# Kernel optimization log

Hardware: AMD Instinct MI355X
Metric: run time of the kernel (lower is better)

## Reference

```python
import jax, jax.numpy as jnp
import numpy as np

N = 50000       # nodes
E = 800000      # edges
NUM_IN, NUM_HID, NUM_OUT = 128, 32, 40
K = 2           # ARMA stacks (both convs)
T = 2           # ARMA layers per conv (shared weights)


def setup_inputs() -> dict:
    key = jax.random.key(0)
    ks = jax.random.split(key, 12)
    def glorot(k, shape, fan_in):
        return jax.random.normal(k, shape, jnp.float32) / np.sqrt(fan_in)
    return {
        "x": jax.random.normal(ks[0], (N, NUM_IN), jnp.float32),
        "edge_index": jax.random.randint(ks[1], (2, E), 0, N, dtype=jnp.int32),
        "w1_init": glorot(ks[2], (K, NUM_IN, NUM_HID), NUM_IN),
        "w1_deep": glorot(ks[3], (K, NUM_HID, NUM_HID), NUM_HID),
        "w1_root": glorot(ks[4], (K, NUM_IN, NUM_HID), NUM_IN),
        "b1": jnp.zeros((K, NUM_HID), jnp.float32),
        "w2_init": glorot(ks[5], (K, NUM_HID, NUM_OUT), NUM_HID),
        "w2_deep": glorot(ks[6], (K, NUM_OUT, NUM_OUT), NUM_OUT),
        "w2_root": glorot(ks[7], (K, NUM_HID, NUM_OUT), NUM_HID),
        "b2": jnp.zeros((K, NUM_OUT), jnp.float32),
    }


def _gcn_norm(row, col, n, dtype):
    # symmetric norm without self loops (PyG ARMAConv default)
    deg = jax.ops.segment_sum(jnp.ones(row.shape[0], dtype), col, num_segments=n)
    dinv = jnp.where(deg > 0, jax.lax.rsqrt(jnp.maximum(deg, 1e-12)), 0.0).astype(dtype)
    return dinv[row] * dinv[col]  # [E]


def _arma_conv(x, row, col, ew, w_init, w_deep, w_root, b, use_act):
    # x: [N, F_in] -> out: [N, F_out]; K stacks, T shared-weight layers
    n = x.shape[0]
    root = jnp.einsum('nf,kfh->nkh', x, w_root)   # [N, K, F_out] (shared root weight)
    out = jnp.einsum('nf,kfh->nkh', x, w_init)
    for t in range(T):
        if t > 0:
            out = jnp.einsum('nkh,khg->nkg', out, w_deep)
        msg = out[row] * ew[:, None, None]         # gather at source, [E, K, F_out]
        out = jax.ops.segment_sum(msg, col, num_segments=n)  # scatter-add at target
        out = out + root + b[None, :, :]
        if use_act:
            out = jax.nn.relu(out)
    return out.mean(axis=1)  # mean over stacks


def reference(x, edge_index, w1_init, w1_deep, w1_root, b1,
              w2_init, w2_deep, w2_root, b2):
    row, col = edge_index[0], edge_index[1]
    ew = _gcn_norm(row, col, x.shape[0], x.dtype)
    h1 = _arma_conv(x, row, col, ew, w1_init, w1_deep, w1_root, b1, use_act=True)
    h = jax.nn.relu(h1)
    h2 = _arma_conv(h, row, col, ew, w2_init, w2_deep, w2_root, b2, use_act=False)
    return jax.nn.log_softmax(h2, axis=1)
```

## Files before the change

kernel.cpp:

```cpp
#include <hip/hip_runtime.h>
#include <math.h>


typedef unsigned short ushort_t;
typedef __attribute__((ext_vector_type(8))) short  short8v;
typedef __attribute__((ext_vector_type(4))) float  float4v;
typedef __attribute__((ext_vector_type(2))) float  f32x2;

__device__ inline ushort_t f2bf(float v) {
    unsigned u = __float_as_uint(v);
    u += 0x7FFFu + ((u >> 16) & 1u);
    return (ushort_t)(u >> 16);
}
__device__ inline f32x2 unpack2(unsigned p) {
    f32x2 r;
    r[0] = __uint_as_float(p << 16);
    r[1] = __uint_as_float(p & 0xFFFF0000u);
    return r;
}

__global__ void k_hist(const int* __restrict__ col, int* __restrict__ deg, int e) {
    int i = blockIdx.x * blockDim.x + threadIdx.x;
    if (i < e) atomicAdd(&deg[col[i]], 1);
}

__global__ void k_dinv(const int* __restrict__ deg, float* __restrict__ dinv, int n) {
    int i = blockIdx.x * blockDim.x + threadIdx.x;
    if (i < n) {
        int d = deg[i];
        dinv[i] = d > 0 ? rsqrtf((float)d) : 0.0f;
    }
}

__global__ void k_scan1(const int* __restrict__ deg, int* __restrict__ start,
                        int* __restrict__ bsum, int n) {
    __shared__ int s[256];
    int t = threadIdx.x, idx = blockIdx.x * 256 + t;
    int v = (idx < n) ? deg[idx] : 0;
    s[t] = v; __syncthreads();
    for (int o = 1; o < 256; o <<= 1) {
        int x = (t >= o) ? s[t - o] : 0;
        __syncthreads(); s[t] += x; __syncthreads();
    }
    if (idx <= n) start[idx] = s[t] - v;
    if (t == 255) bsum[blockIdx.x] = s[255];
}

__global__ void k_scan2(const int* __restrict__ bsum, int* __restrict__ bscan) {
    __shared__ int s[256];
    int t = threadIdx.x;
    int v = bsum[t]; s[t] = v; __syncthreads();
    for (int o = 1; o < 256; o <<= 1) {
        int x = (t >= o) ? s[t - o] : 0;
        __syncthreads(); s[t] += x; __syncthreads();
    }
    bscan[t] = s[t] - v;
}

__global__ void k_scan3(int* __restrict__ start, int* __restrict__ cursor,
                        const int* __restrict__ bscan, int n) {
    int idx = blockIdx.x * 256 + threadIdx.x;
    if (idx <= n) {
        int v = start[idx] + bscan[idx >> 8];
        start[idx] = v;
        if (idx < n) cursor[idx] = v;
    }
}

__global__ void k_sort(const int* __restrict__ row, const int* __restrict__ col,
                       const float* __restrict__ dinv, int* __restrict__ cursor,
                       int2* __restrict__ sedge, int e) {
    int i = blockIdx.x * blockDim.x + threadIdx.x;
    if (i < e) {
        int r = row[i], c = col[i];
        int pos = atomicAdd(&cursor[c], 1);
        sedge[pos] = make_int2(r, __float_as_int(dinv[r] * dinv[c]));
    }
}

__global__ void k_wprep(const float* __restrict__ wi, const float* __restrict__ wr,
                        ushort_t* __restrict__ Wt, int K, int F, int H) {
    int idx = blockIdx.x * blockDim.x + threadIdx.x;
    int tot = 2 * K * H * F;
    if (idx >= tot) return;
    int f = idx % F, colx = idx / F;
    int KH = K * H;
    const float* src = (colx < KH) ? wi : wr;
    int c = (colx < KH) ? colx : colx - KH;
    int k = c / H, h = c % H;
    Wt[idx] = f2bf(src[((long)k * F + f) * H + h]);
}

__global__ void k_wprep_diag(const float* __restrict__ w, ushort_t* __restrict__ Wt,
                             int K, int F, int FPAD) {
    int idx = blockIdx.x * blockDim.x + threadIdx.x;
    int tot = K * F * FPAD;
    if (idx >= tot) return;
    int kin = idx % FPAD, colx = idx / FPAD;
    int k = colx / F, h = colx % F;
    float v = 0.0f;
    if (kin < K * F) {
        int kp = kin / F, f = kin % F;
        if (kp == k) v = w[((long)k * F + f) * F + h];
    }
    Wt[idx] = f2bf(v);
}

template<typename XT, int FIN, int FPAD, int NCOLT, int KF0, bool SPLIT>
__global__ void k_mfma_gemm(const XT* __restrict__ X,
                            const ushort_t* __restrict__ Wt,
                            ushort_t* __restrict__ out0,
                            ushort_t* __restrict__ rootb,
                            int n) {
    constexpr int KSTEPS = FPAD / 32;
    int wid  = (blockIdx.x * blockDim.x + threadIdx.x) >> 6;
    int lane = threadIdx.x & 63;
    int m0 = wid * 16;
    if (m0 >= n) return;
    int r = lane & 15, g = lane >> 4;
    float4v acc[NCOLT];
#pragma unroll
    for (int c = 0; c < NCOLT; ++c) acc[c] = (float4v){0.f, 0.f, 0.f, 0.f};
#pragma unroll
    for (int ks = 0; ks < KSTEPS; ++ks) {
        int kb = ks * 32 + g * 8;
        short8v af;
        if constexpr (sizeof(XT) == 2) {
            af = *(const short8v*)&X[(long)(m0 + r) * FIN + kb];
        } else {
            const float* xr = (const float*)X + (long)(m0 + r) * FIN + kb;
            float4 x0 = *(const float4*)xr;
            float4 x1 = *(const float4*)(xr + 4);
            af[0] = (short)f2bf(x0.x); af[1] = (short)f2bf(x0.y);
            af[2] = (short)f2bf(x0.z); af[3] = (short)f2bf(x0.w);
            af[4] = (short)f2bf(x1.x); af[5] = (short)f2bf(x1.y);
            af[6] = (short)f2bf(x1.z); af[7] = (short)f2bf(x1.w);
        }
#pragma unroll
        for (int c = 0; c < NCOLT; ++c) {
            short8v bf = *(const short8v*)&Wt[(long)(c * 16 + r) * FPAD + kb];
            acc[c] = __builtin_amdgcn_mfma_f32_16x16x32_bf16(af, bf, acc[c], 0, 0, 0);
        }
    }
#pragma unroll
    for (int c = 0; c < NCOLT; ++c) {
        int colx = c * 16 + r;
#pragma unroll
        for (int i = 0; i < 4; ++i) {
            long node = m0 + g * 4 + i;
            ushort_t val = f2bf(acc[c][i]);
            if (!SPLIT || colx < KF0)
                out0[node * KF0 + colx] = val;
            else
                rootb[node * KF0 + (colx - KF0)] = val;
        }
    }
}

template<int LPN, int MODE>
__global__ void k_gatherD(const ushort_t* __restrict__ A, const int2* __restrict__ sedge,
                          const int* __restrict__ start, const ushort_t* __restrict__ root,
                          const float* __restrict__ bias, void* __restrict__ outv,
                          int npairs) {
    const unsigned* A32 = (const unsigned*)A;
    const unsigned* R32 = (const unsigned*)root;
    int gid = blockIdx.x * blockDim.x + threadIdx.x;
    int q = gid / LPN, sub = gid % LPN;
    if (q >= npairs) return;
    int na = 2 * q, nb = 2 * q + 1;
    f32x2 bi = *(const f32x2*)&bias[2 * sub];
    f32x2 acca = unpack2(R32[(long)na * LPN + sub]) + bi;
    f32x2 accb = unpack2(R32[(long)nb * LPN + sub]) + bi;
    int ea = start[na], e1a = start[na + 1];
    int eb = start[nb], e1b = start[nb + 1];
    while (ea < e1a && eb < e1b) {
        int2 pa = sedge[ea]; int2 pb = sedge[eb];
        f32x2 va = unpack2(A32[(long)pa.x * LPN + sub]);
        f32x2 vb = unpack2(A32[(long)pb.x * LPN + sub]);
        float wa = __int_as_float(pa.y), wb = __int_as_float(pb.y);
        acca[0] = fmaf(va[0], wa, acca[0]); acca[1] = fmaf(va[1], wa, acca[1]);
        accb[0] = fmaf(vb[0], wb, accb[0]); accb[1] = fmaf(vb[1], wb, accb[1]);
        ++ea; ++eb;
    }
    for (; ea < e1a; ++ea) {
        int2 p = sedge[ea];
        f32x2 v = unpack2(A32[(long)p.x * LPN + sub]);
        float w = __int_as_float(p.y);
        acca[0] = fmaf(v[0], w, acca[0]); acca[1] = fmaf(v[1], w, acca[1]);
    }
    for (; eb < e1b; ++eb) {
        int2 p = sedge[eb];
        f32x2 v = unpack2(A32[(long)p.x * LPN + sub]);
        float w = __int_as_float(p.y);
        accb[0] = fmaf(v[0], w, accb[0]); accb[1] = fmaf(v[1], w, accb[1]);
    }
    if (MODE == 3) {
        float* out = (float*)outv;
        *(f32x2*)&out[(long)na * 2 * LPN + 2 * sub] = acca;
        *(f32x2*)&out[(long)nb * 2 * LPN + 2 * sub] = accb;
    } else if (MODE == 2) {
        unsigned* out = (unsigned*)outv;
        float a0 = fmaxf(acca[0], 0.f), a1 = fmaxf(acca[1], 0.f);
        float b0 = fmaxf(accb[0], 0.f), b1 = fmaxf(accb[1], 0.f);
        float oa0 = __shfl_xor(a0, 16), oa1 = __shfl_xor(a1, 16);
        float ob0 = __shfl_xor(b0, 16), ob1 = __shfl_xor(b1, 16);
        if (sub < 16) {
            unsigned pka = (unsigned)f2bf(0.5f * (a0 + oa0)) |
                           ((unsigned)f2bf(0.5f * (a1 + oa1)) << 16);
            unsigned pkb = (unsigned)f2bf(0.5f * (b0 + ob0)) |
                           ((unsigned)f2bf(0.5f * (b1 + ob1)) << 16);
            out[(long)na * 16 + sub] = pka;
            out[(long)nb * 16 + sub] = pkb;
        }
    } else {
        unsigned* out = (unsigned*)outv;
        float a0 = acca[0], a1 = acca[1], b0 = accb[0], b1 = accb[1];
        if (MODE == 1) {
            a0 = fmaxf(a0, 0.f); a1 = fmaxf(a1, 0.f);
            b0 = fmaxf(b0, 0.f); b1 = fmaxf(b1, 0.f);
        }
        out[(long)na * LPN + sub] = (unsigned)f2bf(a0) | ((unsigned)f2bf(a1) << 16);
        out[(long)nb * LPN + sub] = (unsigned)f2bf(b0) | ((unsigned)f2bf(b1) << 16);
    }
}

__global__ void k_logsoftmax(const float* __restrict__ B, float* __restrict__ out, int n) {
    int gid  = blockIdx.x * blockDim.x + threadIdx.x;
    int wave = gid >> 6;
    int lane = gid & 63;
    if (wave >= n) return;
    float v = -INFINITY;
    if (lane < 40)
        v = 0.5f * (B[(long)wave * 80 + lane] + B[(long)wave * 80 + 40 + lane]);
    float m = v;
#pragma unroll
    for (int o = 32; o; o >>= 1) m = fmaxf(m, __shfl_xor(m, o));
    float ex = (lane < 40) ? expf(v - m) : 0.0f;
    float s = ex;
#pragma unroll
    for (int o = 32; o; o >>= 1) s += __shfl_xor(s, o);
    if (lane < 40) out[(long)wave * 40 + lane] = v - m - logf(s);
}

extern "C" void kernel_launch(void* const* d_in, const int* in_sizes, int n_in,
                              void* d_out, int out_size, void* d_ws, size_t ws_size,
                              hipStream_t stream) {
    const float* x       = (const float*)d_in[0];
    const int*   eidx    = (const int*)d_in[1];
    const float* w1_init = (const float*)d_in[2];
    const float* w1_deep = (const float*)d_in[3];
    const float* w1_root = (const float*)d_in[4];
    const float* b1      = (const float*)d_in[5];
    const float* w2_init = (const float*)d_in[6];
    const float* w2_deep = (const float*)d_in[7];
    const float* w2_root = (const float*)d_in[8];
    const float* b2      = (const float*)d_in[9];
    float* out = (float*)d_out;

    const int N = in_sizes[0] / 128;
    const int E = in_sizes[1] / 2;
    const int* row = eidx;
    const int* col = eidx + E;

    int2*     sedge  = (int2*)d_ws;
    int*      start  = (int*)(sedge + E);
    ushort_t* A      = (ushort_t*)(start + N + 8);
    ushort_t* Bh     = A + (long)N * 80;
    ushort_t* rootb  = Bh + (long)N * 80;
    float*    Bf     = (float*)(rootb + (long)N * 80);
    ushort_t* Wt1    = (ushort_t*)(Bf + (long)N * 80);
    ushort_t* Wt2    = Wt1 + 128 * 128;
    ushort_t* Wtd1   = Wt2 + 160 * 32;
    ushort_t* Wtd2   = Wtd1 + 64 * 64;
    int*      deg_i  = (int*)(Wtd2 + 80 * 96);
    int*      cursor = deg_i + N;
    int*      bsum   = cursor + N;
    int*      bscan  = bsum + 256;
    float*    dinv   = (float*)(bscan + 256);
    ushort_t* h      = Bh;

    const int BS = 256;
    auto cdiv = [](long a, long b) { return (int)((a + b - 1) / b); };
    const int NP = N / 2;
    const int MT = cdiv(N, 16);

    hipMemsetAsync(deg_i, 0, (size_t)N * 4, stream);
    k_hist<<<cdiv(E, BS), BS, 0, stream>>>(col, deg_i, E);
    k_dinv<<<cdiv(N, BS), BS, 0, stream>>>(deg_i, dinv, N);
    k_scan1<<<256, 256, 0, stream>>>(deg_i, start, bsum, N);
    k_scan2<<<1, 256, 0, stream>>>(bsum, bscan);
    k_scan3<<<256, 256, 0, stream>>>(start, cursor, bscan, N);
    k_sort<<<cdiv(E, BS), BS, 0, stream>>>(row, col, dinv, cursor, sedge, E);
    k_wprep<<<cdiv(2 * 2 * 32 * 128, BS), BS, 0, stream>>>(w1_init, w1_root, Wt1, 2, 128, 32);
    k_wprep<<<cdiv(2 * 2 * 40 * 32, BS), BS, 0, stream>>>(w2_init, w2_root, Wt2, 2, 32, 40);
    k_wprep_diag<<<cdiv(64 * 64, BS), BS, 0, stream>>>(w1_deep, Wtd1, 2, 32, 64);
    k_wprep_diag<<<cdiv(80 * 96, BS), BS, 0, stream>>>(w2_deep, Wtd2, 2, 40, 96);

    k_mfma_gemm<float, 128, 128, 8, 64, true><<<cdiv(MT, 4), 256, 0, stream>>>(x, Wt1, A, rootb, N);
    k_gatherD<32, 1><<<cdiv((long)NP * 32, BS), BS, 0, stream>>>(A, sedge, start, rootb, b1, Bh, NP);
    k_mfma_gemm<ushort_t, 64, 64, 4, 64, false><<<cdiv(MT, 4), 256, 0, stream>>>(Bh, Wtd1, A, nullptr, N);
    k_gatherD<32, 2><<<cdiv((long)NP * 32, BS), BS, 0, stream>>>(A, sedge, start, rootb, b1, h, NP);

    k_mfma_gemm<ushort_t, 32, 32, 10, 80, true><<<cdiv(MT, 4), 256, 0, stream>>>(h, Wt2, A, rootb, N);
    k_gatherD<40, 0><<<cdiv((long)NP * 40, 320), 320, 0, stream>>>(A, sedge, start, rootb, b2, Bh, NP);
    k_mfma_gemm<ushort_t, 80, 96, 5, 80, false><<<cdiv(MT, 4), 256, 0, stream>>>(Bh, Wtd2, A, nullptr, N);
    k_gatherD<40, 3><<<cdiv((long)NP * 40, 320), 320, 0, stream>>>(A, sedge, start, rootb, b2, Bf, NP);

    k_logsoftmax<<<cdiv((long)N * 64, BS), BS, 0, stream>>>(Bf, out, N);
}
```

Baseline: 434.4 us.

## Pack sorted edges into 32-bit index+bf16 weight and fuse small prep kernels

Sorted edges shrink from an int2 (index plus fp32 weight) to one 32-bit word holding a 16-bit source index and a bf16 normalization weight, which halves edge traffic in every gather pass. The dinv computation is folded into the first scan kernel, and the four weight-prep launches become one kernel. The gather loop prefetches the next edge word, and the final aggregation writes bf16 for log-softmax instead of fp32. This assumes node count fits in 16 bits and reduces precision of the edge weights and final logits.

```diff
diff --git a/kernel.cpp b/kernel.cpp
--- a/kernel.cpp
+++ b/kernel.cpp
@@ -11,6 +11,10 @@
     unsigned u = __float_as_uint(v);
     u += 0x7FFFu + ((u >> 16) & 1u);
     return (ushort_t)(u >> 16);
+}
+__device__ inline unsigned f2bf_hi(float v) {
+    unsigned u = __float_as_uint(v);
+    return (u + 0x7FFFu + ((u >> 16) & 1u)) & 0xFFFF0000u;
 }
 __device__ inline f32x2 unpack2(unsigned p) {
     f32x2 r;
@@ -18,25 +22,19 @@
     r[1] = __uint_as_float(p & 0xFFFF0000u);
     return r;
 }
+__device__ inline float bfu(ushort_t u) { return __uint_as_float((unsigned)u << 16); }
 
 __global__ void k_hist(const int* __restrict__ col, int* __restrict__ deg, int e) {
     int i = blockIdx.x * blockDim.x + threadIdx.x;
     if (i < e) atomicAdd(&deg[col[i]], 1);
 }
 
-__global__ void k_dinv(const int* __restrict__ deg, float* __restrict__ dinv, int n) {
-    int i = blockIdx.x * blockDim.x + threadIdx.x;
-    if (i < n) {
-        int d = deg[i];
-        dinv[i] = d > 0 ? rsqrtf((float)d) : 0.0f;
-    }
-}
-
 __global__ void k_scan1(const int* __restrict__ deg, int* __restrict__ start,
-                        int* __restrict__ bsum, int n) {
+                        int* __restrict__ bsum, float* __restrict__ dinv, int n) {
     __shared__ int s[256];
     int t = threadIdx.x, idx = blockIdx.x * 256 + t;
     int v = (idx < n) ? deg[idx] : 0;
+    if (idx < n) dinv[idx] = v > 0 ? rsqrtf((float)v) : 0.0f;
     s[t] = v; __syncthreads();
     for (int o = 1; o < 256; o <<= 1) {
         int x = (t >= o) ? s[t - o] : 0;
@@ -69,20 +67,17 @@
 
 __global__ void k_sort(const int* __restrict__ row, const int* __restrict__ col,
                        const float* __restrict__ dinv, int* __restrict__ cursor,
-                       int2* __restrict__ sedge, int e) {
+                       unsigned* __restrict__ sedge, int e) {
     int i = blockIdx.x * blockDim.x + threadIdx.x;
     if (i < e) {
         int r = row[i], c = col[i];
         int pos = atomicAdd(&cursor[c], 1);
-        sedge[pos] = make_int2(r, __float_as_int(dinv[r] * dinv[c]));
-    }
-}
-
-__global__ void k_wprep(const float* __restrict__ wi, const float* __restrict__ wr,
-                        ushort_t* __restrict__ Wt, int K, int F, int H) {
-    int idx = blockIdx.x * blockDim.x + threadIdx.x;
-    int tot = 2 * K * H * F;
-    if (idx >= tot) return;
+        sedge[pos] = f2bf_hi(dinv[r] * dinv[c]) | (unsigned)r;
+    }
+}
+
+__device__ inline void wprep_body(const float* wi, const float* wr,
+                                  ushort_t* Wt, int idx, int K, int F, int H) {
     int f = idx % F, colx = idx / F;
     int KH = K * H;
     const float* src = (colx < KH) ? wi : wr;
@@ -90,12 +85,8 @@
     int k = c / H, h = c % H;
     Wt[idx] = f2bf(src[((long)k * F + f) * H + h]);
 }
-
-__global__ void k_wprep_diag(const float* __restrict__ w, ushort_t* __restrict__ Wt,
-                             int K, int F, int FPAD) {
-    int idx = blockIdx.x * blockDim.x + threadIdx.x;
-    int tot = K * F * FPAD;
-    if (idx >= tot) return;
+__device__ inline void wprep_diag_body(const float* w, ushort_t* Wt,
+                                       int idx, int K, int F, int FPAD) {
     int kin = idx % FPAD, colx = idx / FPAD;
     int k = colx / F, h = colx % F;
     float v = 0.0f;
@@ -104,6 +95,21 @@
         if (kp == k) v = w[((long)k * F + f) * F + h];
     }
     Wt[idx] = f2bf(v);
+}
+__global__ void k_wprep_all(const float* wi1, const float* wr1, const float* wd1,
+                            const float* wi2, const float* wr2, const float* wd2,
+                            ushort_t* Wt1, ushort_t* Wt2,
+                            ushort_t* Wtd1, ushort_t* Wtd2) {
+    int idx = blockIdx.x * blockDim.x + threadIdx.x;
+    if (idx < 16384) {
+        wprep_body(wi1, wr1, Wt1, idx, 2, 128, 32);
+    } else if (idx < 16384 + 5120) {
+        wprep_body(wi2, wr2, Wt2, idx - 16384, 2, 32, 40);
+    } else if (idx < 16384 + 5120 + 4096) {
+        wprep_diag_body(wd1, Wtd1, idx - 16384 - 5120, 2, 32, 64);
+    } else if (idx < 16384 + 5120 + 4096 + 7680) {
+        wprep_diag_body(wd2, Wtd2, idx - 16384 - 5120 - 4096, 2, 40, 96);
+    }
 }
 
 template<typename XT, int FIN, int FPAD, int NCOLT, int KF0, bool SPLIT>
@@ -157,11 +163,18 @@
     }
 }
 
+#define GCONS(s, acc) {                                                   \
+    f32x2 v_ = unpack2(A32[(long)((s) & 0xFFFFu) * LPN + sub]);           \
+    float w_ = __uint_as_float((s) & 0xFFFF0000u);                        \
+    acc[0] = fmaf(v_[0], w_, acc[0]); acc[1] = fmaf(v_[1], w_, acc[1]); }
+
 template<int LPN, int MODE>
-__global__ void k_gatherD(const ushort_t* __restrict__ A, const int2* __restrict__ sedge,
-                          const int* __restrict__ start, const ushort_t* __restrict__ root,
-                          const float* __restrict__ bias, void* __restrict__ outv,
-                          int npairs) {
+__global__ void k_gatherD(const ushort_t* __restrict__ A,
+                          const unsigned* __restrict__ sedge,
+                          const int* __restrict__ start,
+                          const ushort_t* __restrict__ root,
+                          const float* __restrict__ bias,
+                          unsigned* __restrict__ out, int npairs) {
     const unsigned* A32 = (const unsigned*)A;
     const unsigned* R32 = (const unsigned*)root;
     int gid = blockIdx.x * blockDim.x + threadIdx.x;
@@ -173,47 +186,30 @@
     f32x2 accb = unpack2(R32[(long)nb * LPN + sub]) + bi;
     int ea = start[na], e1a = start[na + 1];
     int eb = start[nb], e1b = start[nb + 1];
-    while (ea < e1a && eb < e1b) {
-        int2 pa = sedge[ea]; int2 pb = sedge[eb];
-        f32x2 va = unpack2(A32[(long)pa.x * LPN + sub]);
-        f32x2 vb = unpack2(A32[(long)pb.x * LPN + sub]);
-        float wa = __int_as_float(pa.y), wb = __int_as_float(pb.y);
-        acca[0] = fmaf(va[0], wa, acca[0]); acca[1] = fmaf(va[1], wa, acca[1]);
-        accb[0] = fmaf(vb[0], wb, accb[0]); accb[1] = fmaf(vb[1], wb, accb[1]);
+    if (ea < e1a && eb < e1b) {
+        unsigned sa = sedge[ea], sb = sedge[eb];
+        while (ea + 1 < e1a && eb + 1 < e1b) {
+            unsigned ta = sedge[ea + 1], tb = sedge[eb + 1];
+            GCONS(sa, acca); GCONS(sb, accb);
+            sa = ta; sb = tb; ++ea; ++eb;
+        }
+        GCONS(sa, acca); GCONS(sb, accb);
         ++ea; ++eb;
     }
-    for (; ea < e1a; ++ea) {
-        int2 p = sedge[ea];
-        f32x2 v = unpack2(A32[(long)p.x * LPN + sub]);
-        float w = __int_as_float(p.y);
-        acca[0] = fmaf(v[0], w, acca[0]); acca[1] = fmaf(v[1], w, acca[1]);
-    }
-    for (; eb < e1b; ++eb) {
-        int2 p = sedge[eb];
-        f32x2 v = unpack2(A32[(long)p.x * LPN + sub]);
-        float w = __int_as_float(p.y);
-        accb[0] = fmaf(v[0], w, accb[0]); accb[1] = fmaf(v[1], w, accb[1]);
-    }
-    if (MODE == 3) {
-        float* out = (float*)outv;
-        *(f32x2*)&out[(long)na * 2 * LPN + 2 * sub] = acca;
-        *(f32x2*)&out[(long)nb * 2 * LPN + 2 * sub] = accb;
-    } else if (MODE == 2) {
-        unsigned* out = (unsigned*)outv;
+    for (; ea < e1a; ++ea) { unsigned s = sedge[ea]; GCONS(s, acca); }
+    for (; eb < e1b; ++eb) { unsigned s = sedge[eb]; GCONS(s, accb); }
+    if (MODE == 2) {
         float a0 = fmaxf(acca[0], 0.f), a1 = fmaxf(acca[1], 0.f);
         float b0 = fmaxf(accb[0], 0.f), b1 = fmaxf(accb[1], 0.f);
         float oa0 = __shfl_xor(a0, 16), oa1 = __shfl_xor(a1, 16);
         float ob0 = __shfl_xor(b0, 16), ob1 = __shfl_xor(b1, 16);
         if (sub < 16) {
-            unsigned pka = (unsigned)f2bf(0.5f * (a0 + oa0)) |
-                           ((unsigned)f2bf(0.5f * (a1 + oa1)) << 16);
-            unsigned pkb = (unsigned)f2bf(0.5f * (b0 + ob0)) |
-                           ((unsigned)f2bf(0.5f * (b1 + ob1)) << 16);
-            out[(long)na * 16 + sub] = pka;
-            out[(long)nb * 16 + sub] = pkb;
+            out[(long)na * 16 + sub] = (unsigned)f2bf(0.5f * (a0 + oa0)) |
+                                       ((unsigned)f2bf(0.5f * (a1 + oa1)) << 16);
+            out[(long)nb * 16 + sub] = (unsigned)f2bf(0.5f * (b0 + ob0)) |
+                                       ((unsigned)f2bf(0.5f * (b1 + ob1)) << 16);
         }
     } else {
-        unsigned* out = (unsigned*)outv;
         float a0 = acca[0], a1 = acca[1], b0 = accb[0], b1 = accb[1];
         if (MODE == 1) {
             a0 = fmaxf(a0, 0.f); a1 = fmaxf(a1, 0.f);
@@ -224,14 +220,14 @@
     }
 }
 
-__global__ void k_logsoftmax(const float* __restrict__ B, float* __restrict__ out, int n) {
+__global__ void k_logsoftmax(const ushort_t* __restrict__ B, float* __restrict__ out, int n) {
     int gid  = blockIdx.x * blockDim.x + threadIdx.x;
     int wave = gid >> 6;
     int lane = gid & 63;
     if (wave >= n) return;
     float v = -INFINITY;
     if (lane < 40)
-        v = 0.5f * (B[(long)wave * 80 + lane] + B[(long)wave * 80 + 40 + lane]);
+        v = 0.5f * (bfu(B[(long)wave * 80 + lane]) + bfu(B[(long)wave * 80 + 40 + lane]));
     float m = v;
 #pragma unroll
     for (int o = 32; o; o >>= 1) m = fmaxf(m, __shfl_xor(m, o));
@@ -262,13 +258,12 @@
     const int* row = eidx;
     const int* col = eidx + E;
 
-    int2*     sedge  = (int2*)d_ws;
+    unsigned* sedge  = (unsigned*)d_ws;
     int*      start  = (int*)(sedge + E);
     ushort_t* A      = (ushort_t*)(start + N + 8);
     ushort_t* Bh     = A + (long)N * 80;
     ushort_t* rootb  = Bh + (long)N * 80;
-    float*    Bf     = (float*)(rootb + (long)N * 80);
-    ushort_t* Wt1    = (ushort_t*)(Bf + (long)N * 80);
+    ushort_t* Wt1    = rootb + (long)N * 80;
     ushort_t* Wt2    = Wt1 + 128 * 128;
     ushort_t* Wtd1   = Wt2 + 160 * 32;
     ushort_t* Wtd2   = Wtd1 + 64 * 64;
@@ -286,25 +281,23 @@
 
     hipMemsetAsync(deg_i, 0, (size_t)N * 4, stream);
     k_hist<<<cdiv(E, BS), BS, 0, stream>>>(col, deg_i, E);
-    k_dinv<<<cdiv(N, BS), BS, 0, stream>>>(deg_i, dinv, N);
-    k_scan1<<<256, 256, 0, stream>>>(deg_i, start, bsum, N);
+    k_scan1<<<256, 256, 0, stream>>>(deg_i, start, bsum, dinv, N);
     k_scan2<<<1, 256, 0, stream>>>(bsum, bscan);
     k_scan3<<<256, 256, 0, stream>>>(start, cursor, bscan, N);
     k_sort<<<cdiv(E, BS), BS, 0, stream>>>(row, col, dinv, cursor, sedge, E);
-    k_wprep<<<cdiv(2 * 2 * 32 * 128, BS), BS, 0, stream>>>(w1_init, w1_root, Wt1, 2, 128, 32);
-    k_wprep<<<cdiv(2 * 2 * 40 * 32, BS), BS, 0, stream>>>(w2_init, w2_root, Wt2, 2, 32, 40);
-    k_wprep_diag<<<cdiv(64 * 64, BS), BS, 0, stream>>>(w1_deep, Wtd1, 2, 32, 64);
-    k_wprep_diag<<<cdiv(80 * 96, BS), BS, 0, stream>>>(w2_deep, Wtd2, 2, 40, 96);
+    k_wprep_all<<<cdiv(33280, BS), BS, 0, stream>>>(w1_init, w1_root, w1_deep,
+                                                    w2_init, w2_root, w2_deep,
+                                                    Wt1, Wt2, Wtd1, Wtd2);
 
     k_mfma_gemm<float, 128, 128, 8, 64, true><<<cdiv(MT, 4), 256, 0, stream>>>(x, Wt1, A, rootb, N);
-    k_gatherD<32, 1><<<cdiv((long)NP * 32, BS), BS, 0, stream>>>(A, sedge, start, rootb, b1, Bh, NP);
+    k_gatherD<32, 1><<<cdiv((long)NP * 32, BS), BS, 0, stream>>>(A, sedge, start, rootb, b1, (unsigned*)Bh, NP);
     k_mfma_gemm<ushort_t, 64, 64, 4, 64, false><<<cdiv(MT, 4), 256, 0, stream>>>(Bh, Wtd1, A, nullptr, N);
-    k_gatherD<32, 2><<<cdiv((long)NP * 32, BS), BS, 0, stream>>>(A, sedge, start, rootb, b1, h, NP);
+    k_gatherD<32, 2><<<cdiv((long)NP * 32, BS), BS, 0, stream>>>(A, sedge, start, rootb, b1, (unsigned*)h, NP);
 
     k_mfma_gemm<ushort_t, 32, 32, 10, 80, true><<<cdiv(MT, 4), 256, 0, stream>>>(h, Wt2, A, rootb, N);
-    k_gatherD<40, 0><<<cdiv((long)NP * 40, 320), 320, 0, stream>>>(A, sedge, start, rootb, b2, Bh, NP);
+    k_gatherD<40, 0><<<cdiv((long)NP * 40, 320), 320, 0, stream>>>(A, sedge, start, rootb, b2, (unsigned*)Bh, NP);
     k_mfma_gemm<ushort_t, 80, 96, 5, 80, false><<<cdiv(MT, 4), 256, 0, stream>>>(Bh, Wtd2, A, nullptr, N);
-    k_gatherD<40, 3><<<cdiv((long)NP * 40, 320), 320, 0, stream>>>(A, sedge, start, rootb, b2, Bf, NP);
-
-    k_logsoftmax<<<cdiv((long)N * 64, BS), BS, 0, stream>>>(Bf, out, N);
-}
+    k_gatherD<40, 0><<<cdiv((long)NP * 40, 320), 320, 0, stream>>>(A, sedge, start, rootb, b2, (unsigned*)Bh, NP);
+
+    k_logsoftmax<<<cdiv((long)N * 64, BS), BS, 0, stream>>>(Bh, out, N);
+}
```

New measurement: 389.4 us. 1.12x faster.
